# Kernel optimization log

Measured on AMD Instinct MI355X. Metric: run time of the kernel, lower is better.

## Reference

```python
import jax, jax.numpy as jnp
import numpy as np


def setup_inputs() -> dict:
    key = jax.random.key(0)
    k1, k2 = jax.random.split(key)
    B, N, C = 32, 1024, 384
    x = jax.random.normal(k1, (B, N, C), dtype=jnp.float32)
    duration = jax.random.randint(k2, (B, N), 0, 8, dtype=jnp.int64)
    return {"x": x, "duration": duration, "max_length": 4096}


def reference(x, duration, max_length):
    # x: [B, N, C], duration: [B, N] int, max_length: python int
    B, N, C = x.shape
    dur = jnp.maximum(duration, 0)                       # duration.clip(min=0)
    cum = jnp.cumsum(dur, axis=1)                        # [B, N] exclusive-end offsets
    total = cum[:, -1]                                   # [B] expanded lengths
    t = jnp.arange(max_length)                           # [L]
    # Output frame t of row b copies token idx where cum[idx-1] <= t < cum[idx]:
    # idx = searchsorted(cum, t, side='right')  (vectorized repeat_interleave gather)
    idx = jax.vmap(lambda c: jnp.searchsorted(c, t, side="right"))(cum)  # [B, L]
    idx = jnp.minimum(idx, N - 1)                        # clamp padding region
    out = jnp.take_along_axis(x, idx[:, :, None], axis=1)  # [B, L, C]
    mel_mask = t[None, :] < total[:, None]               # [B, L] bool
    out = out * mel_mask[:, :, None].astype(x.dtype)     # zero-pad tail (fix_length)
    return out, mel_mask
```

## Files before the change

### kernel.cpp

```cpp
#include <hip/hip_runtime.h>

#define BB 32
#define NN 1024
#define TT 4096
#define CC 384
#define C4 (CC/4)

__global__ void lr_scan_scatter(const int* __restrict__ duration,
                                int* __restrict__ idx_ws) {
    __shared__ int s[NN];
    const int b = blockIdx.x;
    const int n = threadIdx.x;
    int d = duration[b * NN + n];
    if (d < 0) d = 0;
    s[n] = d;
    __syncthreads();
    #pragma unroll
    for (int off = 1; off < NN; off <<= 1) {
        int v = (n >= off) ? s[n - off] : 0;
        __syncthreads();
        s[n] += v;
        __syncthreads();
    }
    int end = s[n];
    int start = end - d;
    if (start < 0) start = 0;
    if (end > TT) end = TT;
    int total = s[NN - 1];
    if (total > TT) total = TT;

    int* row = idx_ws + (size_t)b * TT;
    for (int t = start; t < end; ++t) row[t] = n;
    for (int t = total + n; t < TT; t += NN) row[t] = -1;
}

__global__ void lr_gather(const float4* __restrict__ x4,
                          const int* __restrict__ idx_ws,
                          float4* __restrict__ out4,
                          float* __restrict__ mask) {
    const unsigned total = BB * TT * C4;
    unsigned g = blockIdx.x * blockDim.x + threadIdx.x;
    const unsigned stride = gridDim.x * blockDim.x;
    for (; g < total; g += stride) {
        unsigned row = g / C4;
        unsigned lane = g - row * C4;
        int id = idx_ws[row];
        float4 v = make_float4(0.f, 0.f, 0.f, 0.f);
        if (id >= 0) {
            unsigned b = row >> 12;
            v = x4[((size_t)b * NN + (unsigned)id) * C4 + lane];
        }
        out4[g] = v;
        if (lane == 0) mask[row] = (id >= 0) ? 1.0f : 0.0f;
    }
}

extern "C" void kernel_launch(void* const* d_in, const int* in_sizes, int n_in,
                              void* d_out, int out_size, void* d_ws, size_t ws_size,
                              hipStream_t stream) {
    const float* x        = (const float*)d_in[0];
    const int*   duration = (const int*)d_in[1];

    int*   idx_ws = (int*)d_ws;
    float* out    = (float*)d_out;
    float* mask   = out + (size_t)BB * TT * CC;

    lr_scan_scatter<<<BB, NN, 0, stream>>>(duration, idx_ws);

    lr_gather<<<2048, 256, 0, stream>>>((const float4*)x, idx_ws,
                                        (float4*)out, mask);
}
```

Measured before the change: 53.46 us.

## Fuse scan and gather into one kernel with per-block binary search

Merges the two kernels into one. Each block redoes the duration prefix sum for its batch row using a wave-shuffle scan, then binary-searches the index for each of its 64 output rows and gathers those rows directly. This removes the second launch, the index workspace round trip, and the serial per-thread scatter loop. In exchange, every block repeats the scan of its batch row (64 times per batch), and stores are now nontemporal.

```diff
diff --git a/kernel.cpp b/kernel.cpp
--- a/kernel.cpp
+++ b/kernel.cpp
@@ -5,53 +5,77 @@
 #define TT 4096
 #define CC 384
 #define C4 (CC/4)
+#define RPB 64
+#define BPB (TT/RPB)
+#define THR 256
 
-__global__ void lr_scan_scatter(const int* __restrict__ duration,
-                                int* __restrict__ idx_ws) {
-    __shared__ int s[NN];
-    const int b = blockIdx.x;
-    const int n = threadIdx.x;
-    int d = duration[b * NN + n];
-    if (d < 0) d = 0;
-    s[n] = d;
+typedef float f4v __attribute__((ext_vector_type(4)));
+
+__global__ __launch_bounds__(THR) void lr_fused(const int* __restrict__ duration,
+                                                const float4* __restrict__ x4,
+                                                float4* __restrict__ out4,
+                                                float* __restrict__ mask) {
+    __shared__ int cum[NN];
+    __shared__ int wtot[4];
+    __shared__ int ridx[RPB];
+
+    const int b    = blockIdx.x / BPB;
+    const int rblk = blockIdx.x % BPB;
+    const int tid  = threadIdx.x;
+    const int lane = tid & 63;
+    const int wid  = tid >> 6;
+
+    const int4 dv = ((const int4*)(duration + b * NN))[tid];
+    int d0 = max(dv.x, 0), d1 = max(dv.y, 0), d2 = max(dv.z, 0), d3 = max(dv.w, 0);
+    int p0 = d0, p1 = p0 + d1, p2 = p1 + d2, p3 = p2 + d3;
+
+    int v = p3;
+    #pragma unroll
+    for (int off = 1; off < 64; off <<= 1) {
+        int t = __shfl_up(v, off, 64);
+        if (lane >= off) v += t;
+    }
+    if (lane == 63) wtot[wid] = v;
     __syncthreads();
+    int woff = 0;
     #pragma unroll
-    for (int off = 1; off < NN; off <<= 1) {
-        int v = (n >= off) ? s[n - off] : 0;
-        __syncthreads();
-        s[n] += v;
-        __syncthreads();
+    for (int w = 0; w < 4; ++w)
+        if (w < wid) woff += wtot[w];
+    int excl = woff + (v - p3);
+    int4 cv = make_int4(excl + p0, excl + p1, excl + p2, excl + p3);
+    ((int4*)cum)[tid] = cv;
+    __syncthreads();
+
+    const int total = cum[NN - 1];
+
+    if (tid < RPB) {
+        int row = rblk * RPB + tid;
+        int id = -1;
+        if (row < total) {
+            int lo = 0, hi = NN - 1;
+            #pragma unroll
+            for (int it = 0; it < 10; ++it) {
+                int mid = (lo + hi) >> 1;
+                if (cum[mid] > row) hi = mid; else lo = mid + 1;
+            }
+            id = hi;
+        }
+        ridx[tid] = id;
+        mask[(size_t)b * TT + row] = (id >= 0) ? 1.0f : 0.0f;
     }
-    int end = s[n];
-    int start = end - d;
-    if (start < 0) start = 0;
-    if (end > TT) end = TT;
-    int total = s[NN - 1];
-    if (total > TT) total = TT;
+    __syncthreads();
 
-    int* row = idx_ws + (size_t)b * TT;
-    for (int t = start; t < end; ++t) row[t] = n;
-    for (int t = total + n; t < TT; t += NN) row[t] = -1;
-}
-
-__global__ void lr_gather(const float4* __restrict__ x4,
-                          const int* __restrict__ idx_ws,
-                          float4* __restrict__ out4,
-                          float* __restrict__ mask) {
-    const unsigned total = BB * TT * C4;
-    unsigned g = blockIdx.x * blockDim.x + threadIdx.x;
-    const unsigned stride = gridDim.x * blockDim.x;
-    for (; g < total; g += stride) {
-        unsigned row = g / C4;
-        unsigned lane = g - row * C4;
-        int id = idx_ws[row];
-        float4 v = make_float4(0.f, 0.f, 0.f, 0.f);
-        if (id >= 0) {
-            unsigned b = row >> 12;
-            v = x4[((size_t)b * NN + (unsigned)id) * C4 + lane];
-        }
-        out4[g] = v;
-        if (lane == 0) mask[row] = (id >= 0) ? 1.0f : 0.0f;
+    const float4* xb = x4 + (size_t)b * NN * C4;
+    float4* ob = out4 + ((size_t)b * TT + (size_t)rblk * RPB) * C4;
+    #pragma unroll
+    for (int it = 0; it < RPB * C4 / THR; ++it) {
+        int i = it * THR + tid;
+        int r = i / C4;
+        int lane2 = i - r * C4;
+        int id = ridx[r];
+        float4 vv = make_float4(0.f, 0.f, 0.f, 0.f);
+        if (id >= 0) vv = xb[(size_t)id * C4 + lane2];
+        __builtin_nontemporal_store(*(const f4v*)&vv, (f4v*)&ob[i]);
     }
 }
 
@@ -61,12 +85,9 @@
     const float* x        = (const float*)d_in[0];
     const int*   duration = (const int*)d_in[1];
 
-    int*   idx_ws = (int*)d_ws;
-    float* out    = (float*)d_out;
-    float* mask   = out + (size_t)BB * TT * CC;
+    float* out  = (float*)d_out;
+    float* mask = out + (size_t)BB * TT * CC;
 
-    lr_scan_scatter<<<BB, NN, 0, stream>>>(duration, idx_ws);
-
-    lr_gather<<<2048, 256, 0, stream>>>((const float4*)x, idx_ws,
-                                        (float4*)out, mask);
+    lr_fused<<<BB * BPB, THR, 0, stream>>>(duration, (const float4*)x,
+                                           (float4*)out, mask);
 }
```

Measured after the change: 46.78 us. 12.5% less time.
